# Performance work log

Measured on AMD Instinct MI355X. Metric: run time of the kernel, lower is better.

The kernel has to match this reference:

```python
import jax, jax.numpy as jnp
import numpy as np

LOCAL_RANGE = 7  # module default local_range
NUM_HEADS = 8


def setup_inputs() -> dict:
    key = jax.random.key(0)
    k1, k2, k3 = jax.random.split(key, 3)
    B, S, D = 2, 2048, 512
    hidden_states = jax.random.normal(k1, (B, S, D), dtype=jnp.float32)
    scale = 1.0 / (D ** 0.5)
    Wq = jax.random.normal(k2, (D, D), dtype=jnp.float32) * scale
    Wk = jax.random.normal(k3, (D, D), dtype=jnp.float32) * scale
    return {"hidden_states": hidden_states, "Wq": Wq, "Wk": Wk}


def reference(hidden_states, Wq, Wk):
    B, S, D = hidden_states.shape
    H = NUM_HEADS
    dh = D // H
    # inner attention: only attn_weights matter (context_layer is overwritten)
    q = (hidden_states @ Wq).reshape(B, S, H, dh).transpose(0, 2, 1, 3)  # [B,H,S,dh]
    k = (hidden_states @ Wk).reshape(B, S, H, dh).transpose(0, 2, 1, 3)  # [B,H,S,dh]
    scores = jnp.einsum('bhid,bhjd->bhij', q, k) / (dh ** 0.5)          # [B,H,S,S]
    attn_weights = jax.nn.softmax(scores, axis=-1)
    # band-diagonal local mask: |i-j| <= local_range (vectorized form of the python loop)
    idx = jnp.arange(S)
    band = (jnp.abs(idx[:, None] - idx[None, :]) <= LOCAL_RANGE).astype(attn_weights.dtype)  # [S,S]
    local_w = attn_weights * band
    local_w = local_w / (jnp.sum(local_w, axis=-1, keepdims=True) + 1e-6)
    # context = matmul(local_attn_weights, hidden_states): per-head contraction
    context = jnp.einsum('bhij,bjd->bhid', local_w, hidden_states)       # [B,H,S,D]
    return context
```

## Files before the change

kernel.cpp:

```cpp
#include <hip/hip_runtime.h>
#include <hip/hip_bf16.h>
#include <math.h>

#define SEQ   2048
#define DIM   512
#define NH    8
#define DH    64
#define LR    7
#define TI    8
#define NROW  (TI + 2 * LR)

typedef __bf16 bf16_t;
typedef __bf16 bf16x8 __attribute__((ext_vector_type(8)));
typedef float  f32x4  __attribute__((ext_vector_type(4)));

typedef __attribute__((address_space(3))) void  lds_void;
typedef __attribute__((address_space(1))) const void gbl_cvoid;

__global__ __launch_bounds__(256) void prep(
    const float* __restrict__ hs,
    const float* __restrict__ Wq, const float* __restrict__ Wk,
    bf16_t* __restrict__ hsb,
    bf16_t* __restrict__ Wt)
{
    const int tid = threadIdx.x;
    const int bx  = blockIdx.x;

    if (bx < 1024) {
        const size_t base = ((size_t)bx * 256 + tid) * 8;
        const float4 f0 = *(const float4*)(hs + base);
        const float4 f1 = *(const float4*)(hs + base + 4);
        union { bf16_t b[8]; uint4 u; } cv;
        cv.b[0]=(bf16_t)f0.x; cv.b[1]=(bf16_t)f0.y; cv.b[2]=(bf16_t)f0.z; cv.b[3]=(bf16_t)f0.w;
        cv.b[4]=(bf16_t)f1.x; cv.b[5]=(bf16_t)f1.y; cv.b[6]=(bf16_t)f1.z; cv.b[7]=(bf16_t)f1.w;
        *(uint4*)(hsb + base) = cv.u;
        return;
    }

    __shared__ float tile[64][68];
    const int t  = bx - 1024;
    const int k0 = (t & 7) * 64;
    const int n0 = (t >> 3) * 64;
    const float* W = (n0 < DIM) ? Wq : Wk;
    const int nn0 = n0 & (DIM - 1);

    #pragma unroll
    for (int ph = 0; ph < 4; ++ph) {
        const int kk = ph * 16 + (tid >> 4);
        const int nn = (tid & 15) * 4;
        const float4 v = *(const float4*)(W + (size_t)(k0 + kk) * DIM + nn0 + nn);
        tile[kk][nn + 0] = v.x; tile[kk][nn + 1] = v.y;
        tile[kk][nn + 2] = v.z; tile[kk][nn + 3] = v.w;
    }
    __syncthreads();
    #pragma unroll
    for (int ph = 0; ph < 4; ++ph) {
        const int nn = ph * 16 + (tid >> 4);
        const int kk = (tid & 15) * 4;
        union { bf16_t b[4]; ushort4 u; } cv;
        #pragma unroll
        for (int u = 0; u < 4; ++u) cv.b[u] = (bf16_t)tile[kk + u][nn];
        *(ushort4*)(Wt + (size_t)(n0 + nn) * DIM + k0 + kk) = cv.u;
    }
}

__global__ __launch_bounds__(256) void qk_gemm_mfma(
    const bf16_t* __restrict__ A,
    const bf16_t* __restrict__ Bt,
    bf16_t* __restrict__ C)
{
    __shared__ bf16_t As0[64 * 32], As1[64 * 32];
    __shared__ bf16_t Bs0[128 * 32], Bs1[128 * 32];

    const int tid  = threadIdx.x;
    const int wave = tid >> 6;
    const int lane = tid & 63;
    const int l15  = lane & 15;
    const int quad = lane >> 4;
    const int wm   = (wave >> 1) * 32;
    const int wn_  = (wave & 1) * 64;
    const int m0   = blockIdx.x * 64;
    const int n0   = blockIdx.y * 128;

    const int srow = lane >> 2;
    const int scol = (lane & 3) * 8;

    const bf16_t* agp = A  + (size_t)(m0 + wave * 16 + srow) * DIM + scol;
    const bf16_t* bgp = Bt + (size_t)(n0 + wave * 32 + srow) * DIM + scol;
    bf16_t* al0 = As0 + wave * 16 * 32;
    bf16_t* al1 = As1 + wave * 16 * 32;
    bf16_t* bl0 = Bs0 + wave * 32 * 32;
    bf16_t* bl1 = Bs1 + wave * 32 * 32;

    f32x4 acc[2][4] = {};

    for (int k0 = 0; k0 < DIM; k0 += 64) {
        __builtin_amdgcn_global_load_lds((gbl_cvoid*)(agp + k0),      (lds_void*)al0, 16, 0, 0);
        __builtin_amdgcn_global_load_lds((gbl_cvoid*)(agp + k0 + 32), (lds_void*)al1, 16, 0, 0);
        __builtin_amdgcn_global_load_lds((gbl_cvoid*)(bgp + k0),      (lds_void*)bl0, 16, 0, 0);
        __builtin_amdgcn_global_load_lds((gbl_cvoid*)(bgp + k0 + 32), (lds_void*)bl1, 16, 0, 0);
        __builtin_amdgcn_global_load_lds((gbl_cvoid*)(bgp + 16 * DIM + k0),      (lds_void*)(bl0 + 16 * 32), 16, 0, 0);
        __builtin_amdgcn_global_load_lds((gbl_cvoid*)(bgp + 16 * DIM + k0 + 32), (lds_void*)(bl1 + 16 * 32), 16, 0, 0);
        __syncthreads();

        #pragma unroll
        for (int s = 0; s < 2; ++s) {
            const bf16_t* PA = s ? As1 : As0;
            const bf16_t* PB = s ? Bs1 : Bs0;
            bf16x8 af[2], bfv[4];
            #pragma unroll
            for (int mi = 0; mi < 2; ++mi)
                af[mi] = *(const bf16x8*)(PA + (wm + mi * 16 + l15) * 32 + quad * 8);
            #pragma unroll
            for (int ni = 0; ni < 4; ++ni)
                bfv[ni] = *(const bf16x8*)(PB + (wn_ + ni * 16 + l15) * 32 + quad * 8);
            #pragma unroll
            for (int mi = 0; mi < 2; ++mi)
                #pragma unroll
                for (int ni = 0; ni < 4; ++ni)
                    acc[mi][ni] = __builtin_amdgcn_mfma_f32_16x16x32_bf16(
                        af[mi], bfv[ni], acc[mi][ni], 0, 0, 0);
        }
        __syncthreads();
    }

    #pragma unroll
    for (int mi = 0; mi < 2; ++mi) {
        #pragma unroll
        for (int ni = 0; ni < 4; ++ni) {
            const int col = n0 + wn_ + ni * 16 + l15;
            #pragma unroll
            for (int r = 0; r < 4; ++r) {
                const int row = m0 + wm + mi * 16 + quad * 4 + r;
                C[(size_t)row * 1024 + col] = (bf16_t)acc[mi][ni][r];
            }
        }
    }
}

__global__ __launch_bounds__(256) void local_attn4(
    const float* __restrict__ hs,
    const bf16_t* __restrict__ qkb,
    float* __restrict__ out)
{
    __shared__ __align__(16) char uni[49152];
    bf16_t* Qb   = (bf16_t*)uni;
    bf16_t* Kb   = (bf16_t*)(uni + 16384);
    float*  band = (float*)uni;
    __shared__ float sw2[NH][TI][24];
    __shared__ float wn[NH * TI][16];

    const int tid  = threadIdx.x;
    const int wave = tid >> 6;
    const int lane = tid & 63;
    const int l15  = lane & 15;
    const int quad = lane >> 4;
    const int i0   = blockIdx.x * TI;
    const int b    = blockIdx.y;

    for (int r = wave; r < TI; r += 4) {
        const bf16_t* g = qkb + (size_t)(b * SEQ + i0 + r) * 1024 + lane * 8;
        __builtin_amdgcn_global_load_lds((gbl_cvoid*)g, (lds_void*)(Qb + r * DIM), 16, 0, 0);
    }
    for (int r = wave; r < NROW; r += 4) {
        int jg = i0 - LR + r;
        jg = jg < 0 ? 0 : (jg > SEQ - 1 ? SEQ - 1 : jg);
        const bf16_t* g = qkb + (size_t)(b * SEQ + jg) * 1024 + DIM + lane * 8;
        __builtin_amdgcn_global_load_lds((gbl_cvoid*)g, (lds_void*)(Kb + r * DIM), 16, 0, 0);
    }
    __syncthreads();

    #pragma unroll
    for (int hh = 0; hh < 2; ++hh) {
        const int h = wave * 2 + hh;
        f32x4 sacc[2] = {};
        #pragma unroll
        for (int s = 0; s < 2; ++s) {
            const bf16x8 aq = *(const bf16x8*)(Qb + l15 * DIM + h * DH + s * 32 + quad * 8);
            #pragma unroll
            for (int t = 0; t < 2; ++t) {
                const bf16x8 bk = *(const bf16x8*)(Kb + (t * 16 + l15) * DIM + h * DH + s * 32 + quad * 8);
                sacc[t] = __builtin_amdgcn_mfma_f32_16x16x32_bf16(aq, bk, sacc[t], 0, 0, 0);
            }
        }
        #pragma unroll
        for (int t = 0; t < 2; ++t) {
            const int jj = t * 16 + l15;
            if (jj < NROW) {
                #pragma unroll
                for (int r = 0; r < 4; ++r) {
                    const int ii = quad * 4 + r;
                    if (ii < TI) sw2[h][ii][jj] = sacc[t][r] * 0.125f;
                }
            }
        }
    }
    __syncthreads();

    for (int r = wave; r < NROW; r += 4) {
        int jg = i0 - LR + r;
        jg = jg < 0 ? 0 : (jg > SEQ - 1 ? SEQ - 1 : jg);
        const float* g0 = hs + ((size_t)b * SEQ + jg) * DIM + lane * 4;
        __builtin_amdgcn_global_load_lds((gbl_cvoid*)g0,         (lds_void*)(band + r * DIM),       16, 0, 0);
        __builtin_amdgcn_global_load_lds((gbl_cvoid*)(g0 + 256), (lds_void*)(band + r * DIM + 256), 16, 0, 0);
    }

    if (tid < NH * TI) {
        const int h  = tid >> 3;
        const int ii = tid & (TI - 1);
        const int i  = i0 + ii;
        float v[15], m = -1e30f;
        #pragma unroll
        for (int t = 0; t < 15; ++t) {
            const int jg = i - LR + t;
            v[t] = (jg >= 0 && jg < SEQ) ? sw2[h][ii][ii + t] : -1e30f;
            m = fmaxf(m, v[t]);
        }
        float sum = 0.f;
        #pragma unroll
        for (int t = 0; t < 15; ++t) { v[t] = __expf(v[t] - m); sum += v[t]; }
        const float inv = 1.f / sum;
        #pragma unroll
        for (int t = 0; t < 15; ++t) wn[tid][t] = v[t] * inv;
    }
    __syncthreads();

    {
        const int h  = tid >> 5;
        const int iq = (tid >> 4) & 1;
        const int dg = tid & 15;

        float wreg[4][15];
        #pragma unroll
        for (int t = 0; t < 4; ++t) {
            const int pair = h * TI + iq * 4 + t;
            #pragma unroll
            for (int j = 0; j < 15; ++j) wreg[t][j] = wn[pair][j];
        }

        const int r0 = iq * 4;
        float* op = out + ((size_t)(b * NH + h) * SEQ + i0 + iq * 4) * DIM;

        for (int c = 0; c < DIM / 64; ++c) {
            const int dbase = c * 64 + dg * 4;
            float4 a0 = {0,0,0,0}, a1 = {0,0,0,0}, a2 = {0,0,0,0}, a3 = {0,0,0,0};
            #pragma unroll
            for (int rr = 0; rr < 18; ++rr) {
                const float4 v = *(const float4*)&band[(r0 + rr) * DIM + dbase];
                if (rr <= 14) {
                    const float w = wreg[0][rr];
                    a0.x += w * v.x; a0.y += w * v.y; a0.z += w * v.z; a0.w += w * v.w;
                }
                if (rr >= 1 && rr <= 15) {
                    const float w = wreg[1][rr - 1];
                    a1.x += w * v.x; a1.y += w * v.y; a1.z += w * v.z; a1.w += w * v.w;
                }
                if (rr >= 2 && rr <= 16) {
                    const float w = wreg[2][rr - 2];
                    a2.x += w * v.x; a2.y += w * v.y; a2.z += w * v.z; a2.w += w * v.w;
                }
                if (rr >= 3) {
                    const float w = wreg[3][rr - 3];
                    a3.x += w * v.x; a3.y += w * v.y; a3.z += w * v.z; a3.w += w * v.w;
                }
            }
            *(float4*)(op + (size_t)0 * DIM + dbase) = a0;
            *(float4*)(op + (size_t)1 * DIM + dbase) = a1;
            *(float4*)(op + (size_t)2 * DIM + dbase) = a2;
            *(float4*)(op + (size_t)3 * DIM + dbase) = a3;
        }
    }
}

extern "C" void kernel_launch(void* const* d_in, const int* in_sizes, int n_in,
                              void* d_out, int out_size, void* d_ws, size_t ws_size,
                              hipStream_t stream)
{
    const float* hs = (const float*)d_in[0];
    const float* Wq = (const float*)d_in[1];
    const float* Wk = (const float*)d_in[2];
    float* out = (float*)d_out;

    const int B = in_sizes[0] / (SEQ * DIM);
    const int M = B * SEQ;

    bf16_t* hsb = (bf16_t*)d_ws;
    bf16_t* Wt  = (bf16_t*)((char*)d_ws + (4 << 20));
    bf16_t* qkb = (bf16_t*)((char*)d_ws + (5 << 20));

    prep<<<1024 + 128, 256, 0, stream>>>(hs, Wq, Wk, hsb, Wt);
    qk_gemm_mfma<<<dim3(M / 64, 1024 / 128), 256, 0, stream>>>(hsb, Wt, qkb);
    local_attn4<<<dim3(SEQ / TI, B), 256, 0, stream>>>(hs, qkb, out);
}
```

Before: 105.4 us.

## Retile QK GEMM with swizzled LDS and split attention into scores and context kernels

The Q/K projection GEMM moves to 128x128 tiles with a full 128-wide K slab per stage and an XOR-swizzled LDS layout to avoid bank conflicts. Its output is staged through LDS and written with coalesced 16-byte stores. The fused local attention kernel is split in two: one computes the softmax weights into a workspace buffer, and a context kernel splits the hidden dimension in half to double the grid and cut LDS per block. This aims to raise occupancy and parallelism, at the cost of an extra launch and a global round trip for the weights.

```diff
diff --git a/kernel.cpp b/kernel.cpp
--- a/kernel.cpp
+++ b/kernel.cpp
@@ -64,58 +64,53 @@
     }
 }
 
-__global__ __launch_bounds__(256) void qk_gemm_mfma(
+__global__ __launch_bounds__(256) void qk_gemm_v5(
     const bf16_t* __restrict__ A,
     const bf16_t* __restrict__ Bt,
     bf16_t* __restrict__ C)
 {
-    __shared__ bf16_t As0[64 * 32], As1[64 * 32];
-    __shared__ bf16_t Bs0[128 * 32], Bs1[128 * 32];
+    __shared__ bf16_t As[128 * 128];
+    __shared__ bf16_t Bs[128 * 128];
 
     const int tid  = threadIdx.x;
     const int wave = tid >> 6;
     const int lane = tid & 63;
     const int l15  = lane & 15;
     const int quad = lane >> 4;
-    const int wm   = (wave >> 1) * 32;
+    const int wm   = (wave >> 1) * 64;
     const int wn_  = (wave & 1) * 64;
-    const int m0   = blockIdx.x * 64;
+    const int m0   = blockIdx.x * 128;
     const int n0   = blockIdx.y * 128;
 
-    const int srow = lane >> 2;
-    const int scol = (lane & 3) * 8;
-
-    const bf16_t* agp = A  + (size_t)(m0 + wave * 16 + srow) * DIM + scol;
-    const bf16_t* bgp = Bt + (size_t)(n0 + wave * 32 + srow) * DIM + scol;
-    bf16_t* al0 = As0 + wave * 16 * 32;
-    bf16_t* al1 = As1 + wave * 16 * 32;
-    bf16_t* bl0 = Bs0 + wave * 32 * 32;
-    bf16_t* bl1 = Bs1 + wave * 32 * 32;
-
-    f32x4 acc[2][4] = {};
-
-    for (int k0 = 0; k0 < DIM; k0 += 64) {
-        __builtin_amdgcn_global_load_lds((gbl_cvoid*)(agp + k0),      (lds_void*)al0, 16, 0, 0);
-        __builtin_amdgcn_global_load_lds((gbl_cvoid*)(agp + k0 + 32), (lds_void*)al1, 16, 0, 0);
-        __builtin_amdgcn_global_load_lds((gbl_cvoid*)(bgp + k0),      (lds_void*)bl0, 16, 0, 0);
-        __builtin_amdgcn_global_load_lds((gbl_cvoid*)(bgp + k0 + 32), (lds_void*)bl1, 16, 0, 0);
-        __builtin_amdgcn_global_load_lds((gbl_cvoid*)(bgp + 16 * DIM + k0),      (lds_void*)(bl0 + 16 * 32), 16, 0, 0);
-        __builtin_amdgcn_global_load_lds((gbl_cvoid*)(bgp + 16 * DIM + k0 + 32), (lds_void*)(bl1 + 16 * 32), 16, 0, 0);
+    f32x4 acc[4][4] = {};
+
+    for (int kt = 0; kt < 4; ++kt) {
+        const int k0 = kt * 128;
+        #pragma unroll
+        for (int g = 0; g < 8; ++g) {
+            const int ra = wave * 32 + g * 4 + quad;
+            const int cg = (l15 ^ (ra & 15)) * 8;
+            __builtin_amdgcn_global_load_lds(
+                (gbl_cvoid*)(A + (size_t)(m0 + ra) * DIM + k0 + cg),
+                (lds_void*)(As + (wave * 32 + g * 4) * 128), 16, 0, 0);
+            __builtin_amdgcn_global_load_lds(
+                (gbl_cvoid*)(Bt + (size_t)(n0 + ra) * DIM + k0 + cg),
+                (lds_void*)(Bs + (wave * 32 + g * 4) * 128), 16, 0, 0);
+        }
         __syncthreads();
 
         #pragma unroll
-        for (int s = 0; s < 2; ++s) {
-            const bf16_t* PA = s ? As1 : As0;
-            const bf16_t* PB = s ? Bs1 : Bs0;
-            bf16x8 af[2], bfv[4];
-            #pragma unroll
-            for (int mi = 0; mi < 2; ++mi)
-                af[mi] = *(const bf16x8*)(PA + (wm + mi * 16 + l15) * 32 + quad * 8);
+        for (int s = 0; s < 4; ++s) {
+            const int cs = ((s * 4 + quad) ^ l15) * 8;
+            bf16x8 af[4], bfv[4];
+            #pragma unroll
+            for (int mi = 0; mi < 4; ++mi)
+                af[mi] = *(const bf16x8*)(As + (wm + mi * 16 + l15) * 128 + cs);
             #pragma unroll
             for (int ni = 0; ni < 4; ++ni)
-                bfv[ni] = *(const bf16x8*)(PB + (wn_ + ni * 16 + l15) * 32 + quad * 8);
-            #pragma unroll
-            for (int mi = 0; mi < 2; ++mi)
+                bfv[ni] = *(const bf16x8*)(Bs + (wn_ + ni * 16 + l15) * 128 + cs);
+            #pragma unroll
+            for (int mi = 0; mi < 4; ++mi)
                 #pragma unroll
                 for (int ni = 0; ni < 4; ++ni)
                     acc[mi][ni] = __builtin_amdgcn_mfma_f32_16x16x32_bf16(
@@ -124,31 +119,35 @@
         __syncthreads();
     }
 
-    #pragma unroll
-    for (int mi = 0; mi < 2; ++mi) {
-        #pragma unroll
-        for (int ni = 0; ni < 4; ++ni) {
-            const int col = n0 + wn_ + ni * 16 + l15;
-            #pragma unroll
-            for (int r = 0; r < 4; ++r) {
-                const int row = m0 + wm + mi * 16 + quad * 4 + r;
-                C[(size_t)row * 1024 + col] = (bf16_t)acc[mi][ni][r];
-            }
-        }
-    }
-}
-
-__global__ __launch_bounds__(256) void local_attn4(
-    const float* __restrict__ hs,
+    bf16_t* Ct = As;
+    #pragma unroll
+    for (int mi = 0; mi < 4; ++mi)
+        #pragma unroll
+        for (int ni = 0; ni < 4; ++ni)
+            #pragma unroll
+            for (int r = 0; r < 4; ++r)
+                Ct[(wm + mi * 16 + quad * 4 + r) * 128 + wn_ + ni * 16 + l15] =
+                    (bf16_t)acc[mi][ni][r];
+    __syncthreads();
+    #pragma unroll
+    for (int i = 0; i < 8; ++i) {
+        const int idx = i * 256 + tid;
+        const int row = idx >> 4;
+        const int c16 = idx & 15;
+        *(uint4*)(C + (size_t)(m0 + row) * 1024 + n0 + c16 * 8) =
+            *(const uint4*)(Ct + row * 128 + c16 * 8);
+    }
+}
+
+#define QS 520
+
+__global__ __launch_bounds__(256) void scores_k(
     const bf16_t* __restrict__ qkb,
-    float* __restrict__ out)
-{
-    __shared__ __align__(16) char uni[49152];
-    bf16_t* Qb   = (bf16_t*)uni;
-    bf16_t* Kb   = (bf16_t*)(uni + 16384);
-    float*  band = (float*)uni;
+    float* __restrict__ wn_g)
+{
+    __shared__ bf16_t Qb[16 * QS];
+    __shared__ bf16_t Kb[32 * QS];
     __shared__ float sw2[NH][TI][24];
-    __shared__ float wn[NH * TI][16];
 
     const int tid  = threadIdx.x;
     const int wave = tid >> 6;
@@ -160,13 +159,13 @@
 
     for (int r = wave; r < TI; r += 4) {
         const bf16_t* g = qkb + (size_t)(b * SEQ + i0 + r) * 1024 + lane * 8;
-        __builtin_amdgcn_global_load_lds((gbl_cvoid*)g, (lds_void*)(Qb + r * DIM), 16, 0, 0);
+        __builtin_amdgcn_global_load_lds((gbl_cvoid*)g, (lds_void*)(Qb + r * QS), 16, 0, 0);
     }
     for (int r = wave; r < NROW; r += 4) {
         int jg = i0 - LR + r;
         jg = jg < 0 ? 0 : (jg > SEQ - 1 ? SEQ - 1 : jg);
         const bf16_t* g = qkb + (size_t)(b * SEQ + jg) * 1024 + DIM + lane * 8;
-        __builtin_amdgcn_global_load_lds((gbl_cvoid*)g, (lds_void*)(Kb + r * DIM), 16, 0, 0);
+        __builtin_amdgcn_global_load_lds((gbl_cvoid*)g, (lds_void*)(Kb + r * QS), 16, 0, 0);
     }
     __syncthreads();
 
@@ -176,10 +175,10 @@
         f32x4 sacc[2] = {};
         #pragma unroll
         for (int s = 0; s < 2; ++s) {
-            const bf16x8 aq = *(const bf16x8*)(Qb + l15 * DIM + h * DH + s * 32 + quad * 8);
+            const bf16x8 aq = *(const bf16x8*)(Qb + l15 * QS + h * DH + s * 32 + quad * 8);
             #pragma unroll
             for (int t = 0; t < 2; ++t) {
-                const bf16x8 bk = *(const bf16x8*)(Kb + (t * 16 + l15) * DIM + h * DH + s * 32 + quad * 8);
+                const bf16x8 bk = *(const bf16x8*)(Kb + (t * 16 + l15) * QS + h * DH + s * 32 + quad * 8);
                 sacc[t] = __builtin_amdgcn_mfma_f32_16x16x32_bf16(aq, bk, sacc[t], 0, 0, 0);
             }
         }
@@ -197,19 +196,11 @@
     }
     __syncthreads();
 
-    for (int r = wave; r < NROW; r += 4) {
-        int jg = i0 - LR + r;
-        jg = jg < 0 ? 0 : (jg > SEQ - 1 ? SEQ - 1 : jg);
-        const float* g0 = hs + ((size_t)b * SEQ + jg) * DIM + lane * 4;
-        __builtin_amdgcn_global_load_lds((gbl_cvoid*)g0,         (lds_void*)(band + r * DIM),       16, 0, 0);
-        __builtin_amdgcn_global_load_lds((gbl_cvoid*)(g0 + 256), (lds_void*)(band + r * DIM + 256), 16, 0, 0);
-    }
-
     if (tid < NH * TI) {
         const int h  = tid >> 3;
         const int ii = tid & (TI - 1);
         const int i  = i0 + ii;
-        float v[15], m = -1e30f;
+        float v[16], m = -1e30f;
         #pragma unroll
         for (int t = 0; t < 15; ++t) {
             const int jg = i - LR + t;
@@ -221,54 +212,87 @@
         for (int t = 0; t < 15; ++t) { v[t] = __expf(v[t] - m); sum += v[t]; }
         const float inv = 1.f / sum;
         #pragma unroll
-        for (int t = 0; t < 15; ++t) wn[tid][t] = v[t] * inv;
-    }
-    __syncthreads();
-
+        for (int t = 0; t < 15; ++t) v[t] *= inv;
+        v[15] = 0.f;
+        float* dst = wn_g + ((size_t)(b * 256 + blockIdx.x) * 64 + tid) * 16;
+        #pragma unroll
+        for (int u = 0; u < 4; ++u)
+            *(float4*)(dst + u * 4) = make_float4(v[u*4], v[u*4+1], v[u*4+2], v[u*4+3]);
+    }
+}
+
+#define BST 260
+
+__global__ __launch_bounds__(256) void context_k(
+    const float* __restrict__ hs,
+    const float* __restrict__ wn_g,
+    float* __restrict__ out)
+{
+    __shared__ float band[NROW * BST];
+    __shared__ float wnl[64 * 16];
+
+    const int tid  = threadIdx.x;
+    const int wave = tid >> 6;
+    const int lane = tid & 63;
+    const int tile = blockIdx.x;
+    const int dh_  = blockIdx.y;
+    const int b    = blockIdx.z;
+    const int i0   = tile * TI;
+
+    for (int r = wave; r < NROW; r += 4) {
+        int jg = i0 - LR + r;
+        jg = jg < 0 ? 0 : (jg > SEQ - 1 ? SEQ - 1 : jg);
+        const float* g = hs + ((size_t)b * SEQ + jg) * DIM + dh_ * 256 + lane * 4;
+        __builtin_amdgcn_global_load_lds((gbl_cvoid*)g, (lds_void*)(band + r * BST), 16, 0, 0);
+    }
     {
-        const int h  = tid >> 5;
-        const int iq = (tid >> 4) & 1;
-        const int dg = tid & 15;
-
-        float wreg[4][15];
-        #pragma unroll
-        for (int t = 0; t < 4; ++t) {
-            const int pair = h * TI + iq * 4 + t;
-            #pragma unroll
-            for (int j = 0; j < 15; ++j) wreg[t][j] = wn[pair][j];
-        }
-
-        const int r0 = iq * 4;
-        float* op = out + ((size_t)(b * NH + h) * SEQ + i0 + iq * 4) * DIM;
-
-        for (int c = 0; c < DIM / 64; ++c) {
-            const int dbase = c * 64 + dg * 4;
-            float4 a0 = {0,0,0,0}, a1 = {0,0,0,0}, a2 = {0,0,0,0}, a3 = {0,0,0,0};
-            #pragma unroll
-            for (int rr = 0; rr < 18; ++rr) {
-                const float4 v = *(const float4*)&band[(r0 + rr) * DIM + dbase];
-                if (rr <= 14) {
-                    const float w = wreg[0][rr];
-                    a0.x += w * v.x; a0.y += w * v.y; a0.z += w * v.z; a0.w += w * v.w;
-                }
-                if (rr >= 1 && rr <= 15) {
-                    const float w = wreg[1][rr - 1];
-                    a1.x += w * v.x; a1.y += w * v.y; a1.z += w * v.z; a1.w += w * v.w;
-                }
-                if (rr >= 2 && rr <= 16) {
-                    const float w = wreg[2][rr - 2];
-                    a2.x += w * v.x; a2.y += w * v.y; a2.z += w * v.z; a2.w += w * v.w;
-                }
-                if (rr >= 3) {
-                    const float w = wreg[3][rr - 3];
-                    a3.x += w * v.x; a3.y += w * v.y; a3.z += w * v.z; a3.w += w * v.w;
-                }
-            }
-            *(float4*)(op + (size_t)0 * DIM + dbase) = a0;
-            *(float4*)(op + (size_t)1 * DIM + dbase) = a1;
-            *(float4*)(op + (size_t)2 * DIM + dbase) = a2;
-            *(float4*)(op + (size_t)3 * DIM + dbase) = a3;
-        }
+        const float* g = wn_g + (size_t)(b * 256 + tile) * 1024 + wave * 256 + lane * 4;
+        __builtin_amdgcn_global_load_lds((gbl_cvoid*)g, (lds_void*)(wnl + wave * 256), 16, 0, 0);
+    }
+    __syncthreads();
+
+    const int h  = tid >> 5;
+    const int iq = (tid >> 4) & 1;
+    const int dg = tid & 15;
+
+    float wreg[4][15];
+    #pragma unroll
+    for (int t = 0; t < 4; ++t) {
+        const int pair = h * TI + iq * 4 + t;
+        #pragma unroll
+        for (int j = 0; j < 15; ++j) wreg[t][j] = wnl[pair * 16 + j];
+    }
+
+    const int r0 = iq * 4;
+    float* op = out + ((size_t)(b * NH + h) * SEQ + i0 + iq * 4) * DIM + dh_ * 256;
+
+    for (int c = 0; c < 4; ++c) {
+        const int dbase = c * 64 + dg * 4;
+        float4 a0 = {0,0,0,0}, a1 = {0,0,0,0}, a2 = {0,0,0,0}, a3 = {0,0,0,0};
+        #pragma unroll
+        for (int rr = 0; rr < 18; ++rr) {
+            const float4 v = *(const float4*)&band[(r0 + rr) * BST + dbase];
+            if (rr <= 14) {
+                const float w = wreg[0][rr];
+                a0.x += w * v.x; a0.y += w * v.y; a0.z += w * v.z; a0.w += w * v.w;
+            }
+            if (rr >= 1 && rr <= 15) {
+                const float w = wreg[1][rr - 1];
+                a1.x += w * v.x; a1.y += w * v.y; a1.z += w * v.z; a1.w += w * v.w;
+            }
+            if (rr >= 2 && rr <= 16) {
+                const float w = wreg[2][rr - 2];
+                a2.x += w * v.x; a2.y += w * v.y; a2.z += w * v.z; a2.w += w * v.w;
+            }
+            if (rr >= 3) {
+                const float w = wreg[3][rr - 3];
+                a3.x += w * v.x; a3.y += w * v.y; a3.z += w * v.z; a3.w += w * v.w;
+            }
+        }
+        *(float4*)(op + (size_t)0 * DIM + dbase) = a0;
+        *(float4*)(op + (size_t)1 * DIM + dbase) = a1;
+        *(float4*)(op + (size_t)2 * DIM + dbase) = a2;
+        *(float4*)(op + (size_t)3 * DIM + dbase) = a3;
     }
 }
 
@@ -284,11 +308,13 @@
     const int B = in_sizes[0] / (SEQ * DIM);
     const int M = B * SEQ;
 
-    bf16_t* hsb = (bf16_t*)d_ws;
-    bf16_t* Wt  = (bf16_t*)((char*)d_ws + (4 << 20));
-    bf16_t* qkb = (bf16_t*)((char*)d_ws + (5 << 20));
+    bf16_t* hsb  = (bf16_t*)d_ws;
+    bf16_t* Wt   = (bf16_t*)((char*)d_ws + (4 << 20));
+    bf16_t* qkb  = (bf16_t*)((char*)d_ws + (5 << 20));
+    float*  wn_g = (float*)((char*)d_ws + (13 << 20));
 
     prep<<<1024 + 128, 256, 0, stream>>>(hs, Wq, Wk, hsb, Wt);
-    qk_gemm_mfma<<<dim3(M / 64, 1024 / 128), 256, 0, stream>>>(hsb, Wt, qkb);
-    local_attn4<<<dim3(SEQ / TI, B), 256, 0, stream>>>(hs, qkb, out);
-}
+    qk_gemm_v5<<<dim3(M / 128, 1024 / 128), 256, 0, stream>>>(hsb, Wt, qkb);
+    scores_k<<<dim3(SEQ / TI, B), 256, 0, stream>>>(qkb, wn_g);
+    context_k<<<dim3(SEQ / TI, 2, B), 256, 0, stream>>>(hs, wn_g, out);
+}
```

New measurement: 109.0 us. 3.4% more time.
